# Performance work log

Measured on AMD Instinct MI355X. Metric: run time of the kernel, lower is better.

The kernel has to match this reference:

```python
import jax, jax.numpy as jnp
import numpy as np

EPS = 1e-5

# The 8 fixed sobel kernels from the original module. Summing convolutions with
# the same input equals one convolution with the summed kernel, so we embed the
# four 3x3 kernels (pad=1) into 5x5 (pad=2) and precombine everything into a
# single depthwise 5x5 kernel (exactly the math of detect_edge_1/2 summed).
_K3 = [
    [[2, 4, 2], [0, 0, 0], [-2, -4, -2]],
    [[4, 2, 0], [2, 0, -2], [0, -2, -4]],
    [[2, 0, -2], [4, 0, -4], [2, 0, -2]],
    [[0, -2, -4], [2, 0, -2], [4, 2, 0]],
]
_K5 = [
    [[0, 0, 0, 0, 0], [0, -2, -4, -2, 0], [-1, -4, 0, 4, 1], [0, 2, 4, 2, 0], [0, 0, 0, 0, 0]],
    [[0, 0, -1, 0, 0], [0, -2, -4, 2, 0], [0, -4, 0, 4, 0], [0, -2, 4, 2, 0], [0, 0, 1, 0, 0]],
    [[0, 0, 1, 0, 0], [0, -2, 4, 2, 0], [0, -4, 0, 4, 0], [0, -2, -4, 2, 0], [0, 0, -1, 0, 0]],
    [[0, 0, 0, 0, 0], [0, 2, 4, 2, 0], [-1, -4, 0, 4, 1], [0, -2, -4, -2, 0], [0, 0, 0, 0, 0]],
]

def _combined_sobel_kernel():
    k = np.zeros((5, 5), dtype=np.float32)
    for k3 in _K3:
        k[1:4, 1:4] += np.asarray(k3, dtype=np.float32)
    for k5 in _K5:
        k += np.asarray(k5, dtype=np.float32)
    return jnp.asarray(k)

SOBEL_K = _combined_sobel_kernel()  # [5,5]


def _conv2d(x, w, b, pad):
    # x: [N,C,H,W], w: [O,I,kh,kw]
    y = jax.lax.conv_general_dilated(
        x, w, window_strides=(1, 1), padding=[(pad, pad), (pad, pad)],
        dimension_numbers=('NCHW', 'OIHW', 'NCHW'))
    return y + b[None, :, None, None]


def _bn_relu(y, gamma, beta):
    # BatchNorm2d in training mode: per-channel batch stats over (N,H,W),
    # biased variance, eps=1e-5.
    m = jnp.mean(y, axis=(0, 2, 3), keepdims=True)
    v = jnp.mean(jnp.square(y - m), axis=(0, 2, 3), keepdims=True)
    yn = (y - m) * jax.lax.rsqrt(v + EPS)
    return jax.nn.relu(yn * gamma[None, :, None, None] + beta[None, :, None, None])


def _single_conv(x, w, b, gamma, beta, pad):
    return _bn_relu(_conv2d(x, w, b, pad), gamma, beta)


def _sobel(x):
    # Fused depthwise conv replacing the per-channel loops over 8 kernels.
    C = x.shape[1]
    w = jnp.broadcast_to(SOBEL_K[None, None], (C, 1, 5, 5))
    return jax.lax.conv_general_dilated(
        x, w, window_strides=(1, 1), padding=[(2, 2), (2, 2)],
        dimension_numbers=('NCHW', 'OIHW', 'NCHW'), feature_group_count=C)


def setup_inputs() -> dict:
    key = jax.random.key(0)
    ks = jax.random.split(key, 16)
    Cin, Cout = 64, 128
    Ch = Cout // 2
    B, H, W = 8, 160, 160
    s = 0.05
    d = {
        'input_f': jax.random.normal(ks[0], (B, Cin, H, W), jnp.float32),
        'w1': jax.random.normal(ks[1], (Cout, Cin, 1, 1), jnp.float32) * s,
        'b1': jnp.zeros((Cout,), jnp.float32),
        'g1': jnp.ones((Cout,), jnp.float32),
        'be1': jnp.zeros((Cout,), jnp.float32),
        'w2': jax.random.normal(ks[2], (Ch, Cout, 3, 3), jnp.float32) * s,
        'b2': jnp.zeros((Ch,), jnp.float32),
        'g2': jnp.ones((Ch,), jnp.float32),
        'be2': jnp.zeros((Ch,), jnp.float32),
        'w3': jax.random.normal(ks[3], (Ch, Ch, 3, 3), jnp.float32) * s,
        'b3': jnp.zeros((Ch,), jnp.float32),
        'g3': jnp.ones((Ch,), jnp.float32),
        'be3': jnp.zeros((Ch,), jnp.float32),
        'w4': jax.random.normal(ks[4], (Ch, Cin, 3, 3), jnp.float32) * s,
        'b4': jnp.zeros((Ch,), jnp.float32),
        'g4': jnp.ones((Ch,), jnp.float32),
        'be4': jnp.zeros((Ch,), jnp.float32),
    }
    return d


def reference(input_f, w1, b1, g1, be1, w2, b2, g2, be2, w3, b3, g3, be3, w4, b4, g4, be4):
    c1 = _single_conv(input_f, w1, b1, g1, be1, pad=0)   # [B,Cout,H,W]
    c2 = _single_conv(c1, w2, b2, g2, be2, pad=1)        # [B,Cout//2,H,W]
    edge = _sobel(c2)                                    # depthwise sobel sum
    c3 = _single_conv(edge, w3, b3, g3, be3, pad=1)
    skip = _single_conv(input_f, w4, b4, g4, be4, pad=1)
    return jnp.concatenate([skip, c3], axis=1)           # [B,Cout,H,W]
```

## Files before the change

### kernel.cpp

```cpp
#include <hip/hip_runtime.h>

typedef unsigned short u16;
typedef unsigned int u32;
typedef __attribute__((ext_vector_type(8))) short bf16x8;
typedef __attribute__((ext_vector_type(4))) float f32x4;

#define WD 160
#define HW 25600
#define NPIXF 204800.0f
#define BNEPS 1e-5f
#define SLOTB 6553600ll
#define BATB  13107200ll

__device__ __forceinline__ float bf2f(u16 u){ return __uint_as_float(((u32)u)<<16); }
__device__ __forceinline__ u16 f2bf(float f){ u32 x=__float_as_uint(f); return (u16)((x + 0x7FFFu + ((x>>16)&1u))>>16); }
__device__ __forceinline__ u32 pack2(float a,float b){ return (u32)f2bf(a) | ((u32)f2bf(b)<<16); }

__device__ __forceinline__ f32x4 MF(bf16x8 a, bf16x8 b, f32x4 c){
  return __builtin_amdgcn_mfma_f32_16x16x32_bf16(a, b, c, 0, 0, 0);
}
__device__ __forceinline__ void gload16(const void* g, void* l){
  __builtin_amdgcn_global_load_lds((const __attribute__((address_space(1))) void*)(g),
                                   (__attribute__((address_space(3))) void*)(l), 16, 0, 0);
}

__global__ __launch_bounds__(256) void k_prepw(
    const float* __restrict__ w1, const float* __restrict__ w2,
    const float* __restrict__ w3, const float* __restrict__ w4,
    u16* __restrict__ wp1, u16* __restrict__ wp2,
    u16* __restrict__ wp3, u16* __restrict__ wp4)
{
  int t = blockIdx.x*256 + threadIdx.x;
  if (t < 8192){
    int i = t&7, oc = (t>>3)&127, kc = (t>>10)&3, icb = t>>12;
    wp1[t] = f2bf(w1[oc*64 + icb*32 + kc*8 + i]);
  }
  int u = t - 8192;
  if (u >= 0 && u < 73728){
    int i = u&7, oc = (u>>3)&63, kc = (u>>9)&3, v = u>>11;
    int icb = (v*57)>>9; int tap = v - icb*9;
    wp2[u] = f2bf(w2[(oc*128 + icb*32 + kc*8 + i)*9 + tap]);
  }
  int u3 = t - (8192+73728);
  if (u3 >= 0 && u3 < 36864){
    int k = u3&31, oc = (u3>>5)&63, v = u3>>11;
    int icb = (v >= 9) ? 1 : 0; int tap = v - icb*9;
    wp3[u3] = f2bf(w3[(oc*64 + icb*32 + k)*9 + tap]);
    wp4[u3] = f2bf(w4[(oc*64 + icb*32 + k)*9 + tap]);
  }
}

__global__ __launch_bounds__(256,2) void k_conv1(
    const float* __restrict__ x, const u16* __restrict__ wp1,
    char* __restrict__ dout, float* __restrict__ stats, int nslot)
{
  __shared__ __align__(16) char Xs[16384];
  const int tid = threadIdx.x, lane = tid&63, w = tid>>6;
  const int l15 = lane&15, kc = lane>>4;
  const int b = blockIdx.y, px0 = blockIdx.x*128;
  const float* xb = x + (size_t)b*64*HW;

#pragma unroll
  for (int q=0; q<4; ++q){
    int s = q*256 + tid;
    int icb = s >> 9, sl = s & 511;
    int cp = sl >> 5, px4 = sl & 31;
    const float* pa = xb + (size_t)(icb*32 + cp*2)*HW + px0 + px4*4;
    float4 va = *(const float4*)pa;
    float4 vb = *(const float4*)(pa + HW);
    float fa[4] = {va.x, va.y, va.z, va.w};
    float fb[4] = {vb.x, vb.y, vb.z, vb.w};
#pragma unroll
    for (int e=0;e<4;++e){
      int px = px4*4+e;
      int phys = icb*8192 + px*64 + (((cp>>2) ^ ((px>>1)&3))<<4) + (cp&3)*4;
      *(u32*)(Xs + phys) = pack2(fa[e], fb[e]);
    }
  }
  __syncthreads();

  f32x4 acc[4][4];
  for (int t=0;t<4;++t) for (int o=0;o<4;++o) acc[t][o] = (f32x4){0.f,0.f,0.f,0.f};
  const int och = (w>>1)*64;
  int a1off[4];
  for (int t=0;t<4;++t){
    int px = (w&1)*64 + t*16 + l15;
    a1off[t] = px*64 + ((kc ^ ((px>>1)&3))<<4);
  }
#pragma unroll
  for (int icb=0; icb<2; ++icb){
    bf16x8 a[4], bw[4];
#pragma unroll
    for (int t=0;t<4;++t) a[t] = *(const bf16x8*)(Xs + icb*8192 + a1off[t]);
#pragma unroll
    for (int o=0;o<4;++o)
      bw[o] = *(const bf16x8*)(wp1 + ((size_t)(icb*4 + kc)*128 + och + o*16 + l15)*8);
#pragma unroll
    for (int t=0;t<4;++t)
#pragma unroll
      for (int o=0;o<4;++o)
        acc[t][o] = MF(a[t], bw[o], acc[t][o]);
  }

  u16* c1 = (u16*)(dout + (size_t)b*BATB);
  float sa[4]={0,0,0,0}, sq[4]={0,0,0,0};
  for (int t=0;t<4;++t){
    int pxb = px0 + (w&1)*64 + t*16 + kc*4;
    for (int o=0;o<4;++o){
      int oc = och + o*16 + l15;
#pragma unroll
      for (int r=0;r<4;++r){
        float v = acc[t][o][r];
        c1[(size_t)(pxb + r)*128 + oc] = f2bf(v);
        sa[o]+=v; sq[o]+=v*v;
      }
    }
  }
  const int slot = (blockIdx.y*gridDim.x + blockIdx.x) & (nslot-1);
  for (int o=0;o<4;++o){
    float s1_=sa[o], s2_=sq[o];
    s1_+=__shfl_xor(s1_,16); s2_+=__shfl_xor(s2_,16);
    s1_+=__shfl_xor(s1_,32); s2_+=__shfl_xor(s2_,32);
    if (lane < 16){
      float* p = stats + ((size_t)slot*128 + och + o*16 + l15)*4;
      atomicAdd(p, s1_); atomicAdd(p+1, s2_);
    }
  }
}

__global__ void k_fold(const float* __restrict__ src, float* __restrict__ dst, int nslot){
  int c = threadIdx.x; if (c >= 128) return;
  float sm=0.f, sq=0.f;
  for (int s=0;s<nslot;++s){ const float* p = src + ((size_t)s*128 + c)*4; sm+=p[0]; sq+=p[1]; }
  dst[c*2] = sm; dst[c*2+1] = sq;
}

__global__ void k_fold23(const float* __restrict__ s2, const float* __restrict__ s3,
                         float* __restrict__ f23, int nslot){
  int t = threadIdx.x;
  const float* src = (t < 128) ? s2 : s3;
  int c = t & 127;
  float sm=0.f, sq=0.f;
  for (int s=0;s<nslot;++s){ const float* p = src + ((size_t)s*128 + c)*4; sm+=p[0]; sq+=p[1]; }
  f23[t*2] = sm; f23[t*2+1] = sq;
}

__global__ __launch_bounds__(256,2) void k_conv2(
    char* __restrict__ dout, const u16* __restrict__ wp2,
    const float* __restrict__ f0, const float* __restrict__ g1,
    const float* __restrict__ be1,
    float* __restrict__ statsO, int nslot)
{
  __shared__ __align__(16) char Xs[21760];
  __shared__ __align__(16) float scbi[128][2];
  const int tid = threadIdx.x, lane = tid&63, w = tid>>6;
  const int l15 = lane&15, kc = lane>>4;
  const int b = blockIdx.z, gx0 = blockIdx.x*32, gy0 = blockIdx.y*8;
  const u16* c1raw = (const u16*)(dout + (size_t)b*BATB);
  u16* raw2 = (u16*)(dout + (size_t)b*BATB + SLOTB);

  if (tid < 128){
    float m = f0[tid*2]/NPIXF;
    float v = f0[tid*2+1]/NPIXF - m*m;
    float sc = g1[tid]*rsqrtf(v + BNEPS);
    scbi[tid][0] = sc; scbi[tid][1] = be1[tid] - m*sc;
  }

  f32x4 acc[4][4];
  for (int t=0;t<4;++t) for (int o=0;o<4;++o) acc[t][o] = (f32x4){0.f,0.f,0.f,0.f};

  int xon[2][3];
  for (int h=0;h<2;++h) for (int dx=0;dx<3;++dx){
    int xi = l15 + h*16 + dx;
    xon[h][dx] = xi*64 + ((kc ^ ((xi>>1)&3))<<4);
  }

  __syncthreads();
  for (int icb=0; icb<4; ++icb){
    if (icb) __syncthreads();
    for (int s = tid; s < 1360; s += 256){
      int p = s>>2, sub = s&3;
      int yy = (int)(((u32)p*241u)>>13);
      int xi = p - yy*34;
      int gy = gy0 - 1 + yy, gx = gx0 - 1 + xi;
      int c = sub ^ ((xi>>1)&3);
      uint4 o4 = make_uint4(0,0,0,0);
      if ((unsigned)gy < 160u && (unsigned)gx < 160u){
        int cb = icb*32 + c*8;
        uint4 q = *(const uint4*)(c1raw + ((size_t)(gy*WD+gx)*128 + cb));
        u32 ww[4] = {q.x,q.y,q.z,q.w};
        u32 ro[4];
#pragma unroll
        for (int j=0;j<4;++j){
          float lo = bf2f((u16)(ww[j]&0xFFFFu)), hi = bf2f((u16)(ww[j]>>16));
          lo = fmaxf(0.f, lo*scbi[cb+2*j][0]   + scbi[cb+2*j][1]);
          hi = fmaxf(0.f, hi*scbi[cb+2*j+1][0] + scbi[cb+2*j+1][1]);
          ro[j] = pack2(lo, hi);
        }
        o4 = make_uint4(ro[0],ro[1],ro[2],ro[3]);
      }
      *(uint4*)(Xs + p*64 + sub*16) = o4;
    }
    __syncthreads();
#pragma unroll
    for (int tap=0; tap<9; ++tap){
      const int dy = tap/3, dx = tap - dy*3;
      bf16x8 a[4], bw[4];
#pragma unroll
      for (int o=0;o<4;++o)
        bw[o] = *(const bf16x8*)(wp2 + ((size_t)((icb*9 + tap)*4 + kc)*64 + o*16 + l15)*8);
#pragma unroll
      for (int t=0;t<4;++t)
        a[t] = *(const bf16x8*)(Xs + (2*w + (t>>1) + dy)*2176 + xon[t&1][dx]);
#pragma unroll
      for (int t=0;t<4;++t)
#pragma unroll
        for (int o=0;o<4;++o)
          acc[t][o] = MF(a[t], bw[o], acc[t][o]);
    }
  }

  float sa[4]={0,0,0,0}, sq[4]={0,0,0,0};
  for (int t=0;t<4;++t){
    int gy = gy0 + 2*w + (t>>1);
    int gxb = gx0 + (t&1)*16 + kc*4;
    for (int o=0;o<4;++o){
      int oc = o*16 + l15;
#pragma unroll
      for (int r=0;r<4;++r){
        float v = acc[t][o][r];
        raw2[(size_t)(gy*WD + gxb + r)*64 + oc] = f2bf(v);
        sa[o]+=v; sq[o]+=v*v;
      }
    }
  }
  int slot = (blockIdx.x + 5*(blockIdx.y + 20*blockIdx.z)) & (nslot-1);
  for (int o=0;o<4;++o){
    float s1_=sa[o], s2_=sq[o];
    s1_+=__shfl_xor(s1_,16); s2_+=__shfl_xor(s2_,16);
    s1_+=__shfl_xor(s1_,32); s2_+=__shfl_xor(s2_,32);
    if (lane<16){
      float* p = statsO + ((size_t)slot*128 + o*16 + l15)*4;
      atomicAdd(p,s1_); atomicAdd(p+1,s2_);
    }
  }
}

__global__ __launch_bounds__(256) void k_sobel(
    char* __restrict__ dout, const float* __restrict__ S1,
    const float* __restrict__ g2, const float* __restrict__ be2,
    u16* __restrict__ edge_base, long ebstride, int nslot)
{
  __shared__ float ascS[8], abiS[8];
  int tid = threadIdx.x;
  int b = blockIdx.z, cb = blockIdx.y;
  if (tid < 64){
    int c = cb*8 + (tid&7);
    float sm=0.f, sq=0.f;
    for (int s = tid>>3; s < nslot; s += 8){
      const float* p = S1 + ((size_t)s*128 + c)*4;
      sm += p[0]; sq += p[1];
    }
    sm += __shfl_xor(sm, 8);  sq += __shfl_xor(sq, 8);
    sm += __shfl_xor(sm, 16); sq += __shfl_xor(sq, 16);
    sm += __shfl_xor(sm, 32); sq += __shfl_xor(sq, 32);
    if (tid < 8){
      float m = sm/NPIXF, v = sq/NPIXF - m*m;
      float sc = g2[c]*rsqrtf(v+BNEPS);
      ascS[tid] = sc; abiS[tid] = be2[c] - m*sc;
    }
  }
  __syncthreads();
  int px = blockIdx.x*256 + tid;
  int y = (int)(((u32)px*52429u)>>23);
  int x = px - y*WD;
  const u16* raw2 = (const u16*)(dout + (size_t)b*BATB + SLOTB);
  u16* edge = edge_base + (size_t)b*ebstride;
  float av[8] = {0,0,0,0,0,0,0,0};
  auto TAP = [&](int dy, int dx, float wt){
    int yy = y+dy, xx = x+dx;
    if ((unsigned)yy>=160u || (unsigned)xx>=160u) return;
    uint4 q = *(const uint4*)(raw2 + ((size_t)(yy*WD+xx)*64 + cb*8));
    u32 ww[4] = {q.x,q.y,q.z,q.w};
#pragma unroll
    for (int j=0;j<4;++j){
      float lo = bf2f((u16)(ww[j]&0xFFFFu)), hi = bf2f((u16)(ww[j]>>16));
      lo = fmaxf(0.f, lo*ascS[2*j]   + abiS[2*j]);
      hi = fmaxf(0.f, hi*ascS[2*j+1] + abiS[2*j+1]);
      av[2*j]   += wt*lo;
      av[2*j+1] += wt*hi;
    }
  };
  TAP(-1,-1,4.f); TAP(-1,0,4.f);
  TAP(0,-2,-2.f); TAP(0,-1,-8.f); TAP(0,1,8.f); TAP(0,2,2.f);
  TAP(1,0,-4.f);  TAP(1,1,-4.f);
  uint4 o;
  o.x = pack2(av[0],av[1]); o.y = pack2(av[2],av[3]);
  o.z = pack2(av[4],av[5]); o.w = pack2(av[6],av[7]);
  *(uint4*)(edge + ((size_t)px*64 + cb*8)) = o;
}

__global__ __launch_bounds__(256,2) void k_conv34(
    char* __restrict__ dout, const float* __restrict__ x,
    const u16* __restrict__ wp3, const u16* __restrict__ wp4,
    float* __restrict__ st3, float* __restrict__ st4,
    const u16* __restrict__ zeros, const u16* __restrict__ edge_base,
    long ebstride, int nslot, int mode)
{
  __shared__ __align__(16) char Xs[24576];
  const int tid = threadIdx.x, lane = tid&63, w = tid>>6;
  const int l15 = lane&15, kc = lane>>4;
  int b, job;
  if (mode == 2){ b = blockIdx.z>>1; job = blockIdx.z&1; }
  else          { b = blockIdx.z;    job = mode; }
  const int gx0 = blockIdx.x*32, gy0 = blockIdx.y*8;
  const u16* wp = job ? wp4 : wp3;
  float* statsO = job ? st4 : st3;
  float* out = job ? (float*)(dout + (size_t)b*BATB)
                   : (float*)(dout + (size_t)b*BATB + SLOTB);
  const float* xb = x + (size_t)b*64*HW;
  const u16* edge = edge_base + (size_t)b*ebstride;

  f32x4 acc[4][4];
  for (int m=0;m<4;++m) for (int t=0;t<4;++t) acc[m][t] = (f32x4){0.f,0.f,0.f,0.f};
  int xon[2][3];
  for (int h=0;h<2;++h) for (int dx=0;dx<3;++dx){
    int xi = l15 + h*16 + dx;
    xon[h][dx] = xi*64 + ((kc ^ ((xi>>1)&3))<<4);
  }

  for (int icb=0; icb<2; ++icb){
    if (icb) __syncthreads();
    if (job){
      for (int s = tid; s < 1600; s += 256){
        int s10 = (int)(((u32)s*6554u)>>16);
        int q = s - s10*10;
        int cp = (int)(((u32)s10*6554u)>>16);
        int yq = s10 - cp*10;
        int gy = gy0 - 1 + yq;
        int gxq = gx0 - 4 + q*4;
        float fa[4] = {0,0,0,0}, fb[4] = {0,0,0,0};
        if ((unsigned)gy < 160u){
          const float* pa = xb + (size_t)(icb*32 + cp*2)*HW + gy*WD + gxq;
          if (gxq >= 0 && gxq + 3 < 160){
            float4 va = *(const float4*)pa;
            float4 vb = *(const float4*)(pa + HW);
            fa[0]=va.x; fa[1]=va.y; fa[2]=va.z; fa[3]=va.w;
            fb[0]=vb.x; fb[1]=vb.y; fb[2]=vb.z; fb[3]=vb.w;
          } else {
#pragma unroll
            for (int e=0;e<4;++e){
              int gx = gxq + e;
              if ((unsigned)gx < 160u){ fa[e] = pa[e]; fb[e] = pa[e + HW]; }
            }
          }
        }
#pragma unroll
        for (int e=0;e<4;++e){
          int xi = gxq + e - (gx0 - 1);
          if ((unsigned)xi < 34u){
            int phys = (yq*34 + xi)*64 + (((cp>>2) ^ ((xi>>1)&3))<<4) + (cp&3)*4;
            *(u32*)(Xs + phys) = pack2(fa[e], fb[e]);
          }
        }
      }
    } else {
      for (int it=0; it<6; ++it){
        int s = it*256 + tid;
        int p = s>>2, sub = s&3;
        int yy = (int)(((u32)p*241u)>>13);
        int xi = p - yy*34;
        int gy = gy0-1+yy, gx = gx0-1+xi;
        int c = sub ^ ((xi>>1)&3);
        const u16* src = zeros + ((tid&63)<<3);
        if (p<340 && (unsigned)gy<160u && (unsigned)gx<160u)
          src = edge + ((size_t)(gy*WD+gx)*64 + icb*32 + c*8);
        gload16(src, Xs + (it*256 + (tid & ~63))*16);
      }
      asm volatile("s_waitcnt vmcnt(0)" ::: "memory");
    }
    __syncthreads();

#pragma unroll
    for (int tap=0; tap<9; ++tap){
      const int dy = tap/3, dx = tap - dy*3;
      bf16x8 a[4], bv[4];
#pragma unroll
      for (int m=0;m<4;++m)
        a[m] = *(const bf16x8*)(wp + ((size_t)((icb*9+tap)*64 + m*16 + l15)*32 + kc*8));
#pragma unroll
      for (int t=0;t<4;++t)
        bv[t] = *(const bf16x8*)(Xs + (2*w + (t>>1) + dy)*2176 + xon[t&1][dx]);
#pragma unroll
      for (int m=0;m<4;++m)
#pragma unroll
        for (int t=0;t<4;++t)
          acc[m][t] = MF(a[m], bv[t], acc[m][t]);
    }
  }

  float sa[4][4], sq[4][4];
  for (int m=0;m<4;++m) for (int r=0;r<4;++r){ sa[m][r]=0.f; sq[m][r]=0.f; }
  for (int m=0;m<4;++m){
    for (int t=0;t<4;++t){
      int gy = gy0 + 2*w + (t>>1);
      int gx = gx0 + (t&1)*16 + l15;
#pragma unroll
      for (int r=0;r<4;++r){
        float v = acc[m][t][r];
        out[(size_t)(m*16 + kc*4 + r)*HW + gy*WD + gx] = v;
        sa[m][r]+=v; sq[m][r]+=v*v;
      }
    }
  }
  int slot = (blockIdx.x + 5*(blockIdx.y + 20*blockIdx.z)) & (nslot-1);
  for (int m=0;m<4;++m)
    for (int r=0;r<4;++r){
      float s1_=sa[m][r], s2_=sq[m][r];
      s1_+=__shfl_xor(s1_,1); s2_+=__shfl_xor(s2_,1);
      s1_+=__shfl_xor(s1_,2); s2_+=__shfl_xor(s2_,2);
      s1_+=__shfl_xor(s1_,4); s2_+=__shfl_xor(s2_,4);
      s1_+=__shfl_xor(s1_,8); s2_+=__shfl_xor(s2_,8);
      if (l15==0){
        float* p = statsO + ((size_t)slot*128 + m*16 + kc*4 + r)*4;
        atomicAdd(p,s1_); atomicAdd(p+1,s2_);
      }
    }
}

__global__ __launch_bounds__(256) void k_bnrelu(
    float* __restrict__ io, const float* __restrict__ f23,
    const float* __restrict__ g3, const float* __restrict__ be3,
    const float* __restrict__ g4, const float* __restrict__ be4)
{
  size_t e = ((size_t)blockIdx.x*256 + threadIdx.x)*8;
  int cg = (int)((e/HW) & 127);
  float* p = io + (size_t)blockIdx.y*3276800 + e;
  float sm,sq,gg,bb;
  if (cg>=64){ int c=cg-64; sm=f23[c*2]; sq=f23[c*2+1]; gg=g3[c]; bb=be3[c]; }
  else       { sm=f23[(128+cg)*2]; sq=f23[(128+cg)*2+1]; gg=g4[cg]; bb=be4[cg]; }
  float m = sm/NPIXF;
  float v = sq/NPIXF - m*m;
  float sc = gg*rsqrtf(v + BNEPS);
  float bi = bb - m*sc;
  float4 a = *(float4*)p;
  float4 bq = *(float4*)(p+4);
  a.x=fmaxf(0.f,a.x*sc+bi); a.y=fmaxf(0.f,a.y*sc+bi);
  a.z=fmaxf(0.f,a.z*sc+bi); a.w=fmaxf(0.f,a.w*sc+bi);
  bq.x=fmaxf(0.f,bq.x*sc+bi); bq.y=fmaxf(0.f,bq.y*sc+bi);
  bq.z=fmaxf(0.f,bq.z*sc+bi); bq.w=fmaxf(0.f,bq.w*sc+bi);
  *(float4*)p = a;
  *(float4*)(p+4) = bq;
}

extern "C" void kernel_launch(void* const* d_in, const int* in_sizes, int n_in,
                              void* d_out, int out_size, void* d_ws, size_t ws_size,
                              hipStream_t stream)
{
  const float* x   = (const float*)d_in[0];
  const float* w1  = (const float*)d_in[1];
  const float* g1  = (const float*)d_in[3];
  const float* be1 = (const float*)d_in[4];
  const float* w2  = (const float*)d_in[5];
  const float* g2  = (const float*)d_in[7];
  const float* be2 = (const float*)d_in[8];
  const float* w3  = (const float*)d_in[9];
  const float* g3  = (const float*)d_in[11];
  const float* be3 = (const float*)d_in[12];
  const float* w4  = (const float*)d_in[13];
  const float* g4  = (const float*)d_in[15];
  const float* be4 = (const float*)d_in[16];
  (void)in_sizes; (void)n_in; (void)out_size;

  int nslot = 32;
  auto need = [&](int ns)->size_t{
    return (size_t)4*ns*128*4*4 + 4096 + (size_t)(8192+73728+36864+36864)*2 + 1024;
  };
  while (nslot > 1 && need(nslot) > ws_size) nslot >>= 1;
  if (need(nslot) > ws_size) return;

  char* ws = (char*)d_ws;
  float* S = (float*)ws;
  size_t stg = (size_t)nslot*128*4;
  float* S0=S, *S1=S+stg, *S2=S+2*stg, *S3=S+3*stg;
  float* F = S + 4*stg;
  u16* wp1 = (u16*)(F + 1024);
  u16* wp2 = wp1 + 8192;
  u16* wp3 = wp2 + 73728;
  u16* wp4 = wp3 + 36864;
  u16* zeros = wp4 + 36864;
  size_t base = need(nslot);
  bool big = (ws_size >= base + 26214400ull);
  u16* edge_base;
  long ebstride;
  if (big){ edge_base = (u16*)(ws + base); ebstride = 64L*HW; }
  else    { edge_base = (u16*)((char*)d_out + 3276800); ebstride = BATB/2; }

  hipMemsetAsync(S, 0, 4*stg*sizeof(float), stream);
  hipMemsetAsync(zeros, 0, 1024, stream);

  k_prepw<<<464, 256, 0, stream>>>(w1, w2, w3, w4, wp1, wp2, wp3, wp4);
  k_conv1<<<dim3(200,8), 256, 0, stream>>>(x, wp1, (char*)d_out, S0, nslot);
  k_fold<<<1, 128, 0, stream>>>(S0, F, nslot);
  k_conv2<<<dim3(5,20,8), 256, 0, stream>>>((char*)d_out, wp2, F, g1, be1, S1, nslot);
  k_sobel<<<dim3(100,8,8), 256, 0, stream>>>((char*)d_out, S1, g2, be2, edge_base, ebstride, nslot);
  if (big){
    k_conv34<<<dim3(5,20,16), 256, 0, stream>>>((char*)d_out, x, wp3, wp4, S2, S3,
                                                zeros, edge_base, ebstride, nslot, 2);
  } else {
    k_conv34<<<dim3(5,20,8), 256, 0, stream>>>((char*)d_out, x, wp3, wp4, S2, S3,
                                               zeros, edge_base, ebstride, nslot, 0);
    k_conv34<<<dim3(5,20,8), 256, 0, stream>>>((char*)d_out, x, wp3, wp4, S2, S3,
                                               zeros, edge_base, ebstride, nslot, 1);
  }
  k_fold23<<<1, 256, 0, stream>>>(S2, S3, F + 256, nslot);
  k_bnrelu<<<dim3(1600,8), 256, 0, stream>>>((float*)d_out, F + 256, g3, be3, g4, be4);
}
```

Baseline: 348.3 us.

## Remap block order, fuse BN fold into conv2, preload both channel halves in conv34

Block indices are permuted so consecutive blocks land on different XCDs/batches, and the slot index follows the new order. The separate fold kernel before conv2 is removed; each conv2 block sums the slot stats itself. conv34 doubles LDS to stage both input-channel halves up front, using a partial vmcnt wait so compute on the first half overlaps the second load. Input staging in conv1 and conv34 switches to per-pixel 16-byte LDS writes, and launch bounds plus setprio around the MFMA loops change occupancy and scheduling. The risks are more redundant stat reads in conv2, higher LDS use in conv34, and register pressure from the raised occupancy targets.

```diff
diff --git a/kernel.cpp b/kernel.cpp
--- a/kernel.cpp
+++ b/kernel.cpp
@@ -50,32 +50,30 @@
   }
 }
 
-__global__ __launch_bounds__(256,2) void k_conv1(
+__global__ __launch_bounds__(256,4) void k_conv1(
     const float* __restrict__ x, const u16* __restrict__ wp1,
     char* __restrict__ dout, float* __restrict__ stats, int nslot)
 {
   __shared__ __align__(16) char Xs[16384];
   const int tid = threadIdx.x, lane = tid&63, w = tid>>6;
   const int l15 = lane&15, kc = lane>>4;
-  const int b = blockIdx.y, px0 = blockIdx.x*128;
+  int flat = blockIdx.x + 200*blockIdx.y;
+  flat = (flat&7)*200 + (flat>>3);
+  const int b = flat/200, bx = flat - b*200;
+  const int px0 = bx*128;
   const float* xb = x + (size_t)b*64*HW;
 
 #pragma unroll
   for (int q=0; q<4; ++q){
     int s = q*256 + tid;
-    int icb = s >> 9, sl = s & 511;
-    int cp = sl >> 5, px4 = sl & 31;
-    const float* pa = xb + (size_t)(icb*32 + cp*2)*HW + px0 + px4*4;
-    float4 va = *(const float4*)pa;
-    float4 vb = *(const float4*)(pa + HW);
-    float fa[4] = {va.x, va.y, va.z, va.w};
-    float fb[4] = {vb.x, vb.y, vb.z, vb.w};
-#pragma unroll
-    for (int e=0;e<4;++e){
-      int px = px4*4+e;
-      int phys = icb*8192 + px*64 + (((cp>>2) ^ ((px>>1)&3))<<4) + (cp&3)*4;
-      *(u32*)(Xs + phys) = pack2(fa[e], fb[e]);
-    }
+    int px = s & 127, ck = (s>>7)&3, icb = s>>9;
+    const float* pb = xb + (size_t)(icb*32 + ck*8)*HW + px0 + px;
+    u32 w4[4];
+#pragma unroll
+    for (int j=0;j<4;++j)
+      w4[j] = pack2(pb[(size_t)(2*j)*HW], pb[(size_t)(2*j+1)*HW]);
+    *(uint4*)(Xs + icb*8192 + px*64 + ((ck ^ ((px>>1)&3))<<4))
+        = make_uint4(w4[0],w4[1],w4[2],w4[3]);
   }
   __syncthreads();
 
@@ -87,6 +85,7 @@
     int px = (w&1)*64 + t*16 + l15;
     a1off[t] = px*64 + ((kc ^ ((px>>1)&3))<<4);
   }
+  __builtin_amdgcn_s_setprio(1);
 #pragma unroll
   for (int icb=0; icb<2; ++icb){
     bf16x8 a[4], bw[4];
@@ -101,6 +100,7 @@
       for (int o=0;o<4;++o)
         acc[t][o] = MF(a[t], bw[o], acc[t][o]);
   }
+  __builtin_amdgcn_s_setprio(0);
 
   u16* c1 = (u16*)(dout + (size_t)b*BATB);
   float sa[4]={0,0,0,0}, sq[4]={0,0,0,0};
@@ -116,7 +116,7 @@
       }
     }
   }
-  const int slot = (blockIdx.y*gridDim.x + blockIdx.x) & (nslot-1);
+  const int slot = flat & (nslot-1);
   for (int o=0;o<4;++o){
     float s1_=sa[o], s2_=sq[o];
     s1_+=__shfl_xor(s1_,16); s2_+=__shfl_xor(s2_,16);
@@ -126,13 +126,6 @@
       atomicAdd(p, s1_); atomicAdd(p+1, s2_);
     }
   }
-}
-
-__global__ void k_fold(const float* __restrict__ src, float* __restrict__ dst, int nslot){
-  int c = threadIdx.x; if (c >= 128) return;
-  float sm=0.f, sq=0.f;
-  for (int s=0;s<nslot;++s){ const float* p = src + ((size_t)s*128 + c)*4; sm+=p[0]; sq+=p[1]; }
-  dst[c*2] = sm; dst[c*2+1] = sq;
 }
 
 __global__ void k_fold23(const float* __restrict__ s2, const float* __restrict__ s3,
@@ -145,9 +138,9 @@
   f23[t*2] = sm; f23[t*2+1] = sq;
 }
 
-__global__ __launch_bounds__(256,2) void k_conv2(
+__global__ __launch_bounds__(256,4) void k_conv2(
     char* __restrict__ dout, const u16* __restrict__ wp2,
-    const float* __restrict__ f0, const float* __restrict__ g1,
+    const float* __restrict__ S0, const float* __restrict__ g1,
     const float* __restrict__ be1,
     float* __restrict__ statsO, int nslot)
 {
@@ -155,13 +148,19 @@
   __shared__ __align__(16) float scbi[128][2];
   const int tid = threadIdx.x, lane = tid&63, w = tid>>6;
   const int l15 = lane&15, kc = lane>>4;
-  const int b = blockIdx.z, gx0 = blockIdx.x*32, gy0 = blockIdx.y*8;
+  int flat = blockIdx.x + 5*(blockIdx.y + 20*blockIdx.z);
+  flat = (flat&7)*100 + (flat>>3);
+  const int b = flat/100; int r100 = flat - b*100;
+  const int by = r100/5, bx = r100 - by*5;
+  const int gx0 = bx*32, gy0 = by*8;
   const u16* c1raw = (const u16*)(dout + (size_t)b*BATB);
   u16* raw2 = (u16*)(dout + (size_t)b*BATB + SLOTB);
 
   if (tid < 128){
-    float m = f0[tid*2]/NPIXF;
-    float v = f0[tid*2+1]/NPIXF - m*m;
+    float sm=0.f, sq=0.f;
+    for (int s=0;s<nslot;++s){ const float* p = S0 + ((size_t)s*128 + tid)*4; sm+=p[0]; sq+=p[1]; }
+    float m = sm/NPIXF;
+    float v = sq/NPIXF - m*m;
     float sc = g1[tid]*rsqrtf(v + BNEPS);
     scbi[tid][0] = sc; scbi[tid][1] = be1[tid] - m*sc;
   }
@@ -202,6 +201,7 @@
       *(uint4*)(Xs + p*64 + sub*16) = o4;
     }
     __syncthreads();
+    __builtin_amdgcn_s_setprio(1);
 #pragma unroll
     for (int tap=0; tap<9; ++tap){
       const int dy = tap/3, dx = tap - dy*3;
@@ -218,6 +218,7 @@
         for (int o=0;o<4;++o)
           acc[t][o] = MF(a[t], bw[o], acc[t][o]);
     }
+    __builtin_amdgcn_s_setprio(0);
   }
 
   float sa[4]={0,0,0,0}, sq[4]={0,0,0,0};
@@ -234,7 +235,7 @@
       }
     }
   }
-  int slot = (blockIdx.x + 5*(blockIdx.y + 20*blockIdx.z)) & (nslot-1);
+  int slot = flat & (nslot-1);
   for (int o=0;o<4;++o){
     float s1_=sa[o], s2_=sq[o];
     s1_+=__shfl_xor(s1_,16); s2_+=__shfl_xor(s2_,16);
@@ -253,7 +254,10 @@
 {
   __shared__ float ascS[8], abiS[8];
   int tid = threadIdx.x;
-  int b = blockIdx.z, cb = blockIdx.y;
+  int flat = blockIdx.x + 100*(blockIdx.y + 8*blockIdx.z);
+  flat = (flat&7)*800 + (flat>>3);
+  int b = flat/800; int r800 = flat - b*800;
+  int cb = r800/100, bxx = r800 - cb*100;
   if (tid < 64){
     int c = cb*8 + (tid&7);
     float sm=0.f, sq=0.f;
@@ -271,7 +275,7 @@
     }
   }
   __syncthreads();
-  int px = blockIdx.x*256 + tid;
+  int px = bxx*256 + tid;
   int y = (int)(((u32)px*52429u)>>23);
   int x = px - y*WD;
   const u16* raw2 = (const u16*)(dout + (size_t)b*BATB + SLOTB);
@@ -300,20 +304,26 @@
   *(uint4*)(edge + ((size_t)px*64 + cb*8)) = o;
 }
 
-__global__ __launch_bounds__(256,2) void k_conv34(
+__global__ __launch_bounds__(256,3) void k_conv34(
     char* __restrict__ dout, const float* __restrict__ x,
     const u16* __restrict__ wp3, const u16* __restrict__ wp4,
     float* __restrict__ st3, float* __restrict__ st4,
     const u16* __restrict__ zeros, const u16* __restrict__ edge_base,
     long ebstride, int nslot, int mode)
 {
-  __shared__ __align__(16) char Xs[24576];
+  __shared__ __align__(16) char Xs[49152];
   const int tid = threadIdx.x, lane = tid&63, w = tid>>6;
   const int l15 = lane&15, kc = lane>>4;
+  int bx, by, bzz, flat;
+  if (mode == 2){
+    flat = blockIdx.x + 5*(blockIdx.y + 20*blockIdx.z);
+    flat = (flat&7)*200 + (flat>>3);
+    bzz = flat/100; int r100 = flat - bzz*100; by = r100/5; bx = r100 - by*5;
+  } else { bx = blockIdx.x; by = blockIdx.y; bzz = blockIdx.z;
+           flat = bx + 5*(by + 20*bzz); }
   int b, job;
-  if (mode == 2){ b = blockIdx.z>>1; job = blockIdx.z&1; }
-  else          { b = blockIdx.z;    job = mode; }
-  const int gx0 = blockIdx.x*32, gy0 = blockIdx.y*8;
+  if (mode == 2){ b = bzz>>1; job = bzz&1; } else { b = bzz; job = mode; }
+  const int gx0 = bx*32, gy0 = by*8;
   const u16* wp = job ? wp4 : wp3;
   float* statsO = job ? st4 : st3;
   float* out = job ? (float*)(dout + (size_t)b*BATB)
@@ -321,50 +331,30 @@
   const float* xb = x + (size_t)b*64*HW;
   const u16* edge = edge_base + (size_t)b*ebstride;
 
-  f32x4 acc[4][4];
-  for (int m=0;m<4;++m) for (int t=0;t<4;++t) acc[m][t] = (f32x4){0.f,0.f,0.f,0.f};
-  int xon[2][3];
-  for (int h=0;h<2;++h) for (int dx=0;dx<3;++dx){
-    int xi = l15 + h*16 + dx;
-    xon[h][dx] = xi*64 + ((kc ^ ((xi>>1)&3))<<4);
-  }
-
-  for (int icb=0; icb<2; ++icb){
-    if (icb) __syncthreads();
-    if (job){
-      for (int s = tid; s < 1600; s += 256){
-        int s10 = (int)(((u32)s*6554u)>>16);
-        int q = s - s10*10;
-        int cp = (int)(((u32)s10*6554u)>>16);
-        int yq = s10 - cp*10;
-        int gy = gy0 - 1 + yq;
-        int gxq = gx0 - 4 + q*4;
-        float fa[4] = {0,0,0,0}, fb[4] = {0,0,0,0};
-        if ((unsigned)gy < 160u){
-          const float* pa = xb + (size_t)(icb*32 + cp*2)*HW + gy*WD + gxq;
-          if (gxq >= 0 && gxq + 3 < 160){
-            float4 va = *(const float4*)pa;
-            float4 vb = *(const float4*)(pa + HW);
-            fa[0]=va.x; fa[1]=va.y; fa[2]=va.z; fa[3]=va.w;
-            fb[0]=vb.x; fb[1]=vb.y; fb[2]=vb.z; fb[3]=vb.w;
-          } else {
-#pragma unroll
-            for (int e=0;e<4;++e){
-              int gx = gxq + e;
-              if ((unsigned)gx < 160u){ fa[e] = pa[e]; fb[e] = pa[e + HW]; }
-            }
-          }
-        }
-#pragma unroll
-        for (int e=0;e<4;++e){
-          int xi = gxq + e - (gx0 - 1);
-          if ((unsigned)xi < 34u){
-            int phys = (yq*34 + xi)*64 + (((cp>>2) ^ ((xi>>1)&3))<<4) + (cp&3)*4;
-            *(u32*)(Xs + phys) = pack2(fa[e], fb[e]);
-          }
-        }
-      }
-    } else {
+  if (job){
+    for (int s = tid; s < 2720; s += 256){
+      int icb = (s >= 1360) ? 1 : 0;
+      int sl = s - icb*1360;
+      int ck = (sl>=680) ? ((sl>=1020)?3:2) : ((sl>=340)?1:0);
+      int pp = sl - ck*340;
+      int yq = (int)(((u32)pp*241u)>>13);
+      int xi = pp - yq*34;
+      int gy = gy0-1+yq, gx = gx0-1+xi;
+      u32 w4[4] = {0,0,0,0};
+      if ((unsigned)gy<160u && (unsigned)gx<160u){
+        const float* pb = xb + (size_t)(icb*32 + ck*8)*HW + gy*WD + gx;
+#pragma unroll
+        for (int j=0;j<4;++j)
+          w4[j] = pack2(pb[(size_t)(2*j)*HW], pb[(size_t)(2*j+1)*HW]);
+      }
+      *(uint4*)(Xs + icb*24576 + pp*64 + ((ck ^ ((xi>>1)&3))<<4))
+          = make_uint4(w4[0],w4[1],w4[2],w4[3]);
+    }
+    __syncthreads();
+  } else {
+#pragma unroll
+    for (int icb=0; icb<2; ++icb)
+#pragma unroll
       for (int it=0; it<6; ++it){
         int s = it*256 + tid;
         int p = s>>2, sub = s&3;
@@ -375,12 +365,23 @@
         const u16* src = zeros + ((tid&63)<<3);
         if (p<340 && (unsigned)gy<160u && (unsigned)gx<160u)
           src = edge + ((size_t)(gy*WD+gx)*64 + icb*32 + c*8);
-        gload16(src, Xs + (it*256 + (tid & ~63))*16);
-      }
-      asm volatile("s_waitcnt vmcnt(0)" ::: "memory");
-    }
-    __syncthreads();
-
+        gload16(src, Xs + icb*24576 + (it*256 + (tid & ~63))*16);
+      }
+    asm volatile("s_waitcnt vmcnt(6)\n\ts_barrier" ::: "memory");
+  }
+
+  f32x4 acc[4][4];
+  for (int m=0;m<4;++m) for (int t=0;t<4;++t) acc[m][t] = (f32x4){0.f,0.f,0.f,0.f};
+  int xon[2][3];
+  for (int h=0;h<2;++h) for (int dx=0;dx<3;++dx){
+    int xi = l15 + h*16 + dx;
+    xon[h][dx] = xi*64 + ((kc ^ ((xi>>1)&3))<<4);
+  }
+
+  for (int icb=0; icb<2; ++icb){
+    if (icb == 1 && job == 0)
+      asm volatile("s_waitcnt vmcnt(0)\n\ts_barrier" ::: "memory");
+    __builtin_amdgcn_s_setprio(1);
 #pragma unroll
     for (int tap=0; tap<9; ++tap){
       const int dy = tap/3, dx = tap - dy*3;
@@ -390,13 +391,14 @@
         a[m] = *(const bf16x8*)(wp + ((size_t)((icb*9+tap)*64 + m*16 + l15)*32 + kc*8));
 #pragma unroll
       for (int t=0;t<4;++t)
-        bv[t] = *(const bf16x8*)(Xs + (2*w + (t>>1) + dy)*2176 + xon[t&1][dx]);
+        bv[t] = *(const bf16x8*)(Xs + icb*24576 + (2*w + (t>>1) + dy)*2176 + xon[t&1][dx]);
 #pragma unroll
       for (int m=0;m<4;++m)
 #pragma unroll
         for (int t=0;t<4;++t)
           acc[m][t] = MF(a[m], bv[t], acc[m][t]);
     }
+    __builtin_amdgcn_s_setprio(0);
   }
 
   float sa[4][4], sq[4][4];
@@ -413,7 +415,7 @@
       }
     }
   }
-  int slot = (blockIdx.x + 5*(blockIdx.y + 20*blockIdx.z)) & (nslot-1);
+  int slot = flat & (nslot-1);
   for (int m=0;m<4;++m)
     for (int r=0;r<4;++r){
       float s1_=sa[m][r], s2_=sq[m][r];
@@ -501,8 +503,7 @@
 
   k_prepw<<<464, 256, 0, stream>>>(w1, w2, w3, w4, wp1, wp2, wp3, wp4);
   k_conv1<<<dim3(200,8), 256, 0, stream>>>(x, wp1, (char*)d_out, S0, nslot);
-  k_fold<<<1, 128, 0, stream>>>(S0, F, nslot);
-  k_conv2<<<dim3(5,20,8), 256, 0, stream>>>((char*)d_out, wp2, F, g1, be1, S1, nslot);
+  k_conv2<<<dim3(5,20,8), 256, 0, stream>>>((char*)d_out, wp2, S0, g1, be1, S1, nslot);
   k_sobel<<<dim3(100,8,8), 256, 0, stream>>>((char*)d_out, S1, g2, be2, edge_base, ebstride, nslot);
   if (big){
     k_conv34<<<dim3(5,20,16), 256, 0, stream>>>((char*)d_out, x, wp3, wp4, S2, S3,
@@ -513,6 +514,6 @@
     k_conv34<<<dim3(5,20,8), 256, 0, stream>>>((char*)d_out, x, wp3, wp4, S2, S3,
                                                zeros, edge_base, ebstride, nslot, 1);
   }
-  k_fold23<<<1, 256, 0, stream>>>(S2, S3, F + 256, nslot);
-  k_bnrelu<<<dim3(1600,8), 256, 0, stream>>>((float*)d_out, F + 256, g3, be3, g4, be4);
-}
+  k_fold23<<<1, 256, 0, stream>>>(S2, S3, F, nslot);
+  k_bnrelu<<<dim3(1600,8), 256, 0, stream>>>((float*)d_out, F, g3, be3, g4, be4);
+}
```

Measured after the change: 359.0 us. 3.1% more time.

## Raise occupancy, swizzle block order, fold stats into conv2, rework conv1 load

Applied to the files above, without the earlier changes.

Launch bounds for conv1 and conv2 go from 2 to 4 blocks per SIMD, which may force register spilling. Block indices are remapped so consecutive blocks spread across batches and atomic slots, which is meant to reduce atomic contention. The separate k_fold launch is removed and each conv2 block now sums the conv1 stat slots itself, trading one launch for redundant per-block reads. conv1's input staging changes from float4 loads to strided scalar loads per channel, with one 16-byte LDS store per thread.

```diff
diff --git a/kernel.cpp b/kernel.cpp
--- a/kernel.cpp
+++ b/kernel.cpp
@@ -50,32 +50,30 @@
   }
 }
 
-__global__ __launch_bounds__(256,2) void k_conv1(
+__global__ __launch_bounds__(256,4) void k_conv1(
     const float* __restrict__ x, const u16* __restrict__ wp1,
     char* __restrict__ dout, float* __restrict__ stats, int nslot)
 {
   __shared__ __align__(16) char Xs[16384];
   const int tid = threadIdx.x, lane = tid&63, w = tid>>6;
   const int l15 = lane&15, kc = lane>>4;
-  const int b = blockIdx.y, px0 = blockIdx.x*128;
+  int flat = blockIdx.x + 200*blockIdx.y;
+  flat = (flat&7)*200 + (flat>>3);
+  const int b = flat/200, bx = flat - b*200;
+  const int px0 = bx*128;
   const float* xb = x + (size_t)b*64*HW;
 
 #pragma unroll
   for (int q=0; q<4; ++q){
     int s = q*256 + tid;
-    int icb = s >> 9, sl = s & 511;
-    int cp = sl >> 5, px4 = sl & 31;
-    const float* pa = xb + (size_t)(icb*32 + cp*2)*HW + px0 + px4*4;
-    float4 va = *(const float4*)pa;
-    float4 vb = *(const float4*)(pa + HW);
-    float fa[4] = {va.x, va.y, va.z, va.w};
-    float fb[4] = {vb.x, vb.y, vb.z, vb.w};
-#pragma unroll
-    for (int e=0;e<4;++e){
-      int px = px4*4+e;
-      int phys = icb*8192 + px*64 + (((cp>>2) ^ ((px>>1)&3))<<4) + (cp&3)*4;
-      *(u32*)(Xs + phys) = pack2(fa[e], fb[e]);
-    }
+    int px = s & 127, ck = (s>>7)&3, icb = s>>9;
+    const float* pb = xb + (size_t)(icb*32 + ck*8)*HW + px0 + px;
+    u32 w4[4];
+#pragma unroll
+    for (int j=0;j<4;++j)
+      w4[j] = pack2(pb[(size_t)(2*j)*HW], pb[(size_t)(2*j+1)*HW]);
+    *(uint4*)(Xs + icb*8192 + px*64 + ((ck ^ ((px>>1)&3))<<4))
+        = make_uint4(w4[0],w4[1],w4[2],w4[3]);
   }
   __syncthreads();
 
@@ -116,7 +114,7 @@
       }
     }
   }
-  const int slot = (blockIdx.y*gridDim.x + blockIdx.x) & (nslot-1);
+  const int slot = flat & (nslot-1);
   for (int o=0;o<4;++o){
     float s1_=sa[o], s2_=sq[o];
     s1_+=__shfl_xor(s1_,16); s2_+=__shfl_xor(s2_,16);
@@ -126,13 +124,6 @@
       atomicAdd(p, s1_); atomicAdd(p+1, s2_);
     }
   }
-}
-
-__global__ void k_fold(const float* __restrict__ src, float* __restrict__ dst, int nslot){
-  int c = threadIdx.x; if (c >= 128) return;
-  float sm=0.f, sq=0.f;
-  for (int s=0;s<nslot;++s){ const float* p = src + ((size_t)s*128 + c)*4; sm+=p[0]; sq+=p[1]; }
-  dst[c*2] = sm; dst[c*2+1] = sq;
 }
 
 __global__ void k_fold23(const float* __restrict__ s2, const float* __restrict__ s3,
@@ -145,9 +136,9 @@
   f23[t*2] = sm; f23[t*2+1] = sq;
 }
 
-__global__ __launch_bounds__(256,2) void k_conv2(
+__global__ __launch_bounds__(256,4) void k_conv2(
     char* __restrict__ dout, const u16* __restrict__ wp2,
-    const float* __restrict__ f0, const float* __restrict__ g1,
+    const float* __restrict__ S0, const float* __restrict__ g1,
     const float* __restrict__ be1,
     float* __restrict__ statsO, int nslot)
 {
@@ -155,13 +146,19 @@
   __shared__ __align__(16) float scbi[128][2];
   const int tid = threadIdx.x, lane = tid&63, w = tid>>6;
   const int l15 = lane&15, kc = lane>>4;
-  const int b = blockIdx.z, gx0 = blockIdx.x*32, gy0 = blockIdx.y*8;
+  int flat = blockIdx.x + 5*(blockIdx.y + 20*blockIdx.z);
+  flat = (flat&7)*100 + (flat>>3);
+  const int b = flat/100; int r100 = flat - b*100;
+  const int by = r100/5, bx = r100 - by*5;
+  const int gx0 = bx*32, gy0 = by*8;
   const u16* c1raw = (const u16*)(dout + (size_t)b*BATB);
   u16* raw2 = (u16*)(dout + (size_t)b*BATB + SLOTB);
 
   if (tid < 128){
-    float m = f0[tid*2]/NPIXF;
-    float v = f0[tid*2+1]/NPIXF - m*m;
+    float sm=0.f, sq=0.f;
+    for (int s=0;s<nslot;++s){ const float* p = S0 + ((size_t)s*128 + tid)*4; sm+=p[0]; sq+=p[1]; }
+    float m = sm/NPIXF;
+    float v = sq/NPIXF - m*m;
     float sc = g1[tid]*rsqrtf(v + BNEPS);
     scbi[tid][0] = sc; scbi[tid][1] = be1[tid] - m*sc;
   }
@@ -234,7 +231,7 @@
       }
     }
   }
-  int slot = (blockIdx.x + 5*(blockIdx.y + 20*blockIdx.z)) & (nslot-1);
+  int slot = flat & (nslot-1);
   for (int o=0;o<4;++o){
     float s1_=sa[o], s2_=sq[o];
     s1_+=__shfl_xor(s1_,16); s2_+=__shfl_xor(s2_,16);
@@ -490,21 +487,20 @@
   u16* wp4 = wp3 + 36864;
   u16* zeros = wp4 + 36864;
   size_t base = need(nslot);
-  bool big = (ws_size >= base + 26214400ull);
-  u16* edge_base;
-  long ebstride;
-  if (big){ edge_base = (u16*)(ws + base); ebstride = 64L*HW; }
-  else    { edge_base = (u16*)((char*)d_out + 3276800); ebstride = BATB/2; }
+  bool bigWS = (ws_size >= base + 26214400ull);
+  u16* edge_base; long ebstride;
+  if (bigWS){ edge_base = (u16*)(ws + base); ebstride = 64L*HW; }
+  else      { edge_base = (u16*)((char*)d_out + 3276800); ebstride = BATB/2; }
 
   hipMemsetAsync(S, 0, 4*stg*sizeof(float), stream);
   hipMemsetAsync(zeros, 0, 1024, stream);
 
   k_prepw<<<464, 256, 0, stream>>>(w1, w2, w3, w4, wp1, wp2, wp3, wp4);
   k_conv1<<<dim3(200,8), 256, 0, stream>>>(x, wp1, (char*)d_out, S0, nslot);
-  k_fold<<<1, 128, 0, stream>>>(S0, F, nslot);
-  k_conv2<<<dim3(5,20,8), 256, 0, stream>>>((char*)d_out, wp2, F, g1, be1, S1, nslot);
-  k_sobel<<<dim3(100,8,8), 256, 0, stream>>>((char*)d_out, S1, g2, be2, edge_base, ebstride, nslot);
-  if (big){
+  k_conv2<<<dim3(5,20,8), 256, 0, stream>>>((char*)d_out, wp2, S0, g1, be1, S1, nslot);
+  k_sobel<<<dim3(100,8,8), 256, 0, stream>>>((char*)d_out, S1, g2, be2,
+                                             edge_base, ebstride, nslot);
+  if (bigWS){
     k_conv34<<<dim3(5,20,16), 256, 0, stream>>>((char*)d_out, x, wp3, wp4, S2, S3,
                                                 zeros, edge_base, ebstride, nslot, 2);
   } else {
@@ -513,6 +509,6 @@
     k_conv34<<<dim3(5,20,8), 256, 0, stream>>>((char*)d_out, x, wp3, wp4, S2, S3,
                                                zeros, edge_base, ebstride, nslot, 1);
   }
-  k_fold23<<<1, 256, 0, stream>>>(S2, S3, F + 256, nslot);
-  k_bnrelu<<<dim3(1600,8), 256, 0, stream>>>((float*)d_out, F + 256, g3, be3, g4, be4);
-}
+  k_fold23<<<1, 256, 0, stream>>>(S2, S3, F, nslot);
+  k_bnrelu<<<dim3(1600,8), 256, 0, stream>>>((float*)d_out, F, g3, be3, g4, be4);
+}
```

After: 341.6 us. About the same (-1.9%).
